# Performance work log

Hardware: AMD Instinct MI355X
Metric: run time of the kernel (lower is better)

The kernel has to match this reference:

```python
import jax, jax.numpy as jnp
import numpy as np

DIM = 1024
NUM_HEAD = 16
N_IMG = 64


def _linear_params(key, scale=0.02):
    kw, kb = jax.random.split(key)
    W = jax.random.normal(kw, (DIM, DIM), jnp.float32) * scale
    b = jax.random.normal(kb, (DIM,), jnp.float32) * scale
    return W, b


def setup_inputs() -> dict:
    key = jax.random.key(0)
    ks = jax.random.split(key, 5)
    # ragged per-image instance counts: 128..254, deterministic, sum = 12224
    lens = (128 + 2 * np.arange(N_IMG)).astype(np.int64)
    N = int(lens.sum())  # 12224
    x = jax.random.normal(ks[0], (N, DIM), jnp.float32)
    Wq, bq = _linear_params(ks[1])
    Wk, bk = _linear_params(ks[2])
    Wv, bv = _linear_params(ks[3])
    Wu, bu = _linear_params(ks[4])
    return {"x": x, "Wq": Wq, "bq": bq, "Wk": Wk, "bk": bk,
            "Wv": Wv, "bv": bv, "Wu": Wu, "bu": bu,
            "num_inst_per_image": jnp.asarray(lens)}


def _segment_layout(num_inst_per_image):
    # static (int) metadata -> numpy; returns padded gather idx, key mask, unpad idx
    lens = np.asarray(num_inst_per_image)
    B = lens.shape[0]
    L = int(lens.max())
    offsets = np.concatenate([[0], np.cumsum(lens)[:-1]])
    pos = offsets[:, None] + np.arange(L)[None, :]           # [B, L] flat positions
    valid = np.arange(L)[None, :] < lens[:, None]            # [B, L]
    gather_idx = jnp.asarray(np.where(valid, pos, 0))        # safe gather
    flat_take = jnp.asarray(np.flatnonzero(valid.ravel()))   # [N] unpad (row-major = segment order)
    return gather_idx, jnp.asarray(valid), flat_take, B, L


def reference(x, Wq, bq, Wk, bk, Wv, bv, Wu, bu, num_inst_per_image):
    gather_idx, valid, flat_take, B, L = _segment_layout(num_inst_per_image)
    N, C = x.shape
    H = NUM_HEAD
    D = C // H
    # global QKV projections on the flat batch (as in the torch module)
    q = (x @ Wq + bq)[gather_idx].reshape(B, L, H, D)
    k = (x @ Wk + bk)[gather_idx].reshape(B, L, H, D)
    v = (x @ Wv + bv)[gather_idx].reshape(B, L, H, D)
    scale = 1.0 / np.sqrt(C)  # note: original divides by sqrt(C), not sqrt(head_dim)
    attn = jnp.einsum('bqhd,bkhd->bhqk', q, k) * scale       # [B, H, L, L]
    bias = jnp.where(valid[:, None, None, :], 0.0, -jnp.inf)  # mask padded keys
    attn = jax.nn.softmax(attn + bias, axis=-1)
    out = jnp.einsum('bhqk,bkhd->bqhd', attn, v).reshape(B * L, C)
    out = out[flat_take]                                      # unpad back to [N, C]
    return out @ Wu + bu
```

## Files before the change

kernel.cpp:

```cpp
#include <hip/hip_runtime.h>
#include <hip/hip_bf16.h>
#include <math.h>

#define DIMC 1024
#define NHEAD 16
#define HDIM 64
#define MPAD 12288

using bf16x8 = __attribute__((ext_vector_type(8))) short;
using f32x4  = __attribute__((ext_vector_type(4))) float;
using f32x16 = __attribute__((ext_vector_type(16))) float;

__device__ inline ushort f2bf(float f) {
    uint u = __float_as_uint(f);
    u += 0x7fffu + ((u >> 16) & 1u);
    return (ushort)(u >> 16);
}
__device__ inline float bf2f(ushort h) { return __uint_as_float(((uint)h) << 16); }

__device__ inline uint pkbf(float a, float b) {
    __hip_bfloat162 t = __float22bfloat162_rn(float2{a, b});
    return *reinterpret_cast<uint*>(&t);
}

__device__ inline void gload_lds16(const ushort* g, ushort* l) {
    __builtin_amdgcn_global_load_lds(
        (const __attribute__((address_space(1))) uint*)g,
        (__attribute__((address_space(3))) uint*)l, 16, 0, 0);
}

__global__ __launch_bounds__(512, 4) void gemm192(
    const ushort* __restrict__ A, const ushort* __restrict__ Bt,
    const float* __restrict__ bq, const float* __restrict__ bk,
    const float* __restrict__ bv,
    ushort* __restrict__ qb, ushort* __restrict__ kb, ushort* __restrict__ vb,
    int M)
{
    __shared__ ushort lds[2][(128 + 192) * 64];

    const int bid = blockIdx.x;
    const int xcd = bid & 7;
    const int j   = bid >> 3;
    const int mt  = xcd * 12 + (j % 12);
    const int nt  = j / 12;
    const int row0 = mt * 128;
    const int col0 = nt * 192;

    const int t512 = threadIdx.x;
    const int w    = t512 >> 6;
    const int lane = t512 & 63;
    const int wm   = w >> 2;
    const int wn   = w & 3;
    const int l15  = lane & 15;
    const int kh   = lane >> 4;

    const int a0row = (w < 4) ? (w * 8) : (64 + (w - 4) * 8);
    const int a1row = a0row + 32;

    auto stage = [&](int buf, int kt, int mat, int relRow) {
        const int o   = relRow * 128 + lane * 16;
        const int row = o >> 7;
        const int kb_ = (o & 127) ^ ((row & 7) << 4);
        const ushort* src = (mat ? Bt + (size_t)(col0 + row) * DIMC
                                 : A  + (size_t)(row0 + row) * DIMC)
                            + kt * 64 + (kb_ >> 1);
        gload_lds16(src, &lds[buf][0] + mat * (128 * 64) + relRow * 64);
    };
    auto rdA = [&](int buf, int rf, int ks) -> bf16x8 {
        const int row = wm * 64 + rf * 16 + l15;
        const int ad  = (row * 128 + ks * 64 + kh * 16) ^ ((row & 7) << 4);
        return *(const bf16x8*)(&lds[buf][0] + (ad >> 1));
    };
    auto rdB = [&](int buf, int n, int ks) -> bf16x8 {
        const int row = wn * 48 + n * 16 + l15;
        const int ad  = (row * 128 + ks * 64 + kh * 16) ^ ((row & 7) << 4);
        return *(const bf16x8*)(&lds[buf][128 * 64] + (ad >> 1));
    };

    f32x4 acc[4][3] = {};
    bf16x8 af[2][2];
    bf16x8 bf[3][2];

    stage(0, 0, 0, a0row);
    stage(0, 0, 1, w * 24);
    stage(0, 0, 1, w * 24 + 8);
    stage(0, 0, 1, w * 24 + 16);
    stage(0, 0, 0, a1row);

    const int NT = DIMC / 64;
    for (int t = 0; t < NT; ++t) {
        const int cur = t & 1;
        const int nxt = cur ^ 1;
        const int tn  = (t + 1 < NT) ? (t + 1) : (NT - 1);

        asm volatile("s_waitcnt vmcnt(1)" ::: "memory");
        __builtin_amdgcn_s_barrier();
        __builtin_amdgcn_sched_barrier(0);
        #pragma unroll
        for (int rf = 0; rf < 2; ++rf)
            #pragma unroll
            for (int ks = 0; ks < 2; ++ks)
                af[rf][ks] = rdA(cur, rf, ks);
        #pragma unroll
        for (int n = 0; n < 3; ++n)
            #pragma unroll
            for (int ks = 0; ks < 2; ++ks)
                bf[n][ks] = rdB(cur, n, ks);
        stage(nxt, tn, 0, a0row);
        stage(nxt, tn, 1, w * 24);
        stage(nxt, tn, 1, w * 24 + 8);
        stage(nxt, tn, 1, w * 24 + 16);
        __builtin_amdgcn_s_setprio(1);
        #pragma unroll
        for (int rf = 0; rf < 2; ++rf)
            #pragma unroll
            for (int n = 0; n < 3; ++n)
                #pragma unroll
                for (int ks = 0; ks < 2; ++ks)
                    acc[rf][n] = __builtin_amdgcn_mfma_f32_16x16x32_bf16(
                        af[rf][ks], bf[n][ks], acc[rf][n], 0, 0, 0);
        __builtin_amdgcn_s_setprio(0);

        asm volatile("s_waitcnt vmcnt(4)" ::: "memory");
        __builtin_amdgcn_s_barrier();
        __builtin_amdgcn_sched_barrier(0);
        #pragma unroll
        for (int rf = 0; rf < 2; ++rf)
            #pragma unroll
            for (int ks = 0; ks < 2; ++ks)
                af[rf][ks] = rdA(cur, 2 + rf, ks);
        stage(nxt, tn, 0, a1row);
        __builtin_amdgcn_s_setprio(1);
        #pragma unroll
        for (int rf = 0; rf < 2; ++rf)
            #pragma unroll
            for (int n = 0; n < 3; ++n)
                #pragma unroll
                for (int ks = 0; ks < 2; ++ks)
                    acc[2 + rf][n] = __builtin_amdgcn_mfma_f32_16x16x32_bf16(
                        af[rf][ks], bf[n][ks], acc[2 + rf][n], 0, 0, 0);
        __builtin_amdgcn_s_setprio(0);
    }

    #pragma unroll
    for (int n = 0; n < 3; ++n) {
        const int cg = col0 + wn * 48 + n * 16 + l15;
        const int s  = cg >> 10;
        const int cb = cg & 1023;
        const float bb = ((s == 0) ? bq : (s == 1) ? bk : bv)[cb];
        ushort* op     = (s == 0) ? qb : (s == 1) ? kb : vb;
        #pragma unroll
        for (int i = 0; i < 4; ++i) {
            #pragma unroll
            for (int r = 0; r < 4; ++r) {
                const int gr = row0 + wm * 64 + i * 16 + kh * 4 + r;
                if (gr < M)
                    op[(size_t)gr * DIMC + cb] = f2bf(acc[i][n][r] + bb);
            }
        }
    }
}

__global__ __launch_bounds__(512, 4) void gemmF(
    const ushort* __restrict__ A, const ushort* __restrict__ Bt,
    const float* __restrict__ bias, float* __restrict__ C, int M)
{
    __shared__ ushort lds[2][(192 + 128) * 64];

    const int bid = blockIdx.x;
    const int xcd = bid & 7;
    const int j   = bid >> 3;
    const int mt  = xcd * 8 + (j % 8);
    const int nt  = j / 8;
    const int row0 = mt * 192;
    const int col0 = nt * 128;

    const int t512 = threadIdx.x;
    const int w    = t512 >> 6;
    const int lane = t512 & 63;
    const int wm   = w >> 1;
    const int wn   = w & 1;
    const int l15  = lane & 15;
    const int kh   = lane >> 4;

    auto stage = [&](int buf, int kt, int mat, int relRow) {
        const int o   = relRow * 128 + lane * 16;
        const int row = o >> 7;
        const int kb_ = (o & 127) ^ ((row & 7) << 4);
        const ushort* src = (mat ? Bt + (size_t)(col0 + row) * DIMC
                                 : A  + (size_t)(row0 + row) * DIMC)
                            + kt * 64 + (kb_ >> 1);
        gload_lds16(src, &lds[buf][0] + mat * (192 * 64) + relRow * 64);
    };
    auto rdA = [&](int buf, int rf, int ks) -> bf16x8 {
        const int row = wm * 48 + rf * 16 + l15;
        const int ad  = (row * 128 + ks * 64 + kh * 16) ^ ((row & 7) << 4);
        return *(const bf16x8*)(&lds[buf][0] + (ad >> 1));
    };
    auto rdB = [&](int buf, int n, int ks) -> bf16x8 {
        const int row = wn * 64 + n * 16 + l15;
        const int ad  = (row * 128 + ks * 64 + kh * 16) ^ ((row & 7) << 4);
        return *(const bf16x8*)(&lds[buf][192 * 64] + (ad >> 1));
    };

    f32x4 acc[3][4] = {};
    bf16x8 af[3][2];
    bf16x8 bf[4][2];

    stage(0, 0, 1, w * 16);
    stage(0, 0, 1, w * 16 + 8);
    stage(0, 0, 0, w * 8);
    stage(0, 0, 0, 64 + w * 8);
    stage(0, 0, 0, 128 + w * 8);

    const int NT = DIMC / 64;
    for (int t = 0; t < NT; ++t) {
        const int cur = t & 1;
        const int nxt = cur ^ 1;
        const int tn  = (t + 1 < NT) ? (t + 1) : (NT - 1);

        asm volatile("s_waitcnt vmcnt(0)" ::: "memory");
        __builtin_amdgcn_s_barrier();
        __builtin_amdgcn_sched_barrier(0);

        #pragma unroll
        for (int rf = 0; rf < 3; ++rf)
            #pragma unroll
            for (int ks = 0; ks < 2; ++ks)
                af[rf][ks] = rdA(cur, rf, ks);
        #pragma unroll
        for (int n = 0; n < 4; ++n)
            #pragma unroll
            for (int ks = 0; ks < 2; ++ks)
                bf[n][ks] = rdB(cur, n, ks);

        stage(nxt, tn, 1, w * 16);
        stage(nxt, tn, 1, w * 16 + 8);
        stage(nxt, tn, 0, w * 8);
        stage(nxt, tn, 0, 64 + w * 8);
        stage(nxt, tn, 0, 128 + w * 8);

        __builtin_amdgcn_s_setprio(1);
        #pragma unroll
        for (int rf = 0; rf < 3; ++rf)
            #pragma unroll
            for (int n = 0; n < 4; ++n)
                #pragma unroll
                for (int ks = 0; ks < 2; ++ks)
                    acc[rf][n] = __builtin_amdgcn_mfma_f32_16x16x32_bf16(
                        af[rf][ks], bf[n][ks], acc[rf][n], 0, 0, 0);
        __builtin_amdgcn_s_setprio(0);
    }

    #pragma unroll
    for (int n = 0; n < 4; ++n) {
        const int c  = col0 + wn * 64 + n * 16 + l15;
        const float bb = bias[c];
        #pragma unroll
        for (int i = 0; i < 3; ++i) {
            #pragma unroll
            for (int r = 0; r < 4; ++r) {
                const int gr = row0 + wm * 48 + i * 16 + kh * 4 + r;
                if (gr < M)
                    C[(size_t)gr * DIMC + c] = acc[i][n][r] + bb;
            }
        }
    }
}

__global__ __launch_bounds__(256) void cvt_pad(
    const float* __restrict__ x, ushort* __restrict__ xb, int nvalid, int ntot)
{
    const int stride = gridDim.x * blockDim.x;
    for (int i = blockIdx.x * blockDim.x + threadIdx.x; i < ntot / 4; i += stride) {
        const int e = i * 4;
        ushort4 o;
        if (e < nvalid) {
            const float4 f = *(const float4*)(x + e);
            o.x = f2bf(f.x); o.y = f2bf(f.y); o.z = f2bf(f.z); o.w = f2bf(f.w);
        } else { o.x = o.y = o.z = o.w = 0; }
        *(ushort4*)(xb + e) = o;
    }
}

__global__ __launch_bounds__(256) void transpose_w4(
    const float* __restrict__ W0, const float* __restrict__ W1,
    const float* __restrict__ W2, const float* __restrict__ W3,
    ushort* __restrict__ T0, ushort* __restrict__ T1,
    ushort* __restrict__ T2, ushort* __restrict__ T3)
{
    __shared__ float tile[32][33];
    const int z = blockIdx.z;
    const float* W = (z == 0) ? W0 : (z == 1) ? W1 : (z == 2) ? W2 : W3;
    ushort*      T = (z == 0) ? T0 : (z == 1) ? T1 : (z == 2) ? T2 : T3;
    const int tx = threadIdx.x & 31;
    const int ty = threadIdx.x >> 5;
    const int n0 = blockIdx.x * 32;
    const int k0 = blockIdx.y * 32;
    #pragma unroll
    for (int i = 0; i < 32; i += 8)
        tile[ty + i][tx] = W[(size_t)(k0 + ty + i) * DIMC + n0 + tx];
    __syncthreads();
    #pragma unroll
    for (int i = 0; i < 32; i += 8)
        T[(size_t)(n0 + ty + i) * DIMC + k0 + tx] = f2bf(tile[tx][ty + i]);
}

__global__ __launch_bounds__(256) void attn_mfma(
    const ushort* __restrict__ qg, const ushort* __restrict__ kg,
    const ushort* __restrict__ vg, ushort* __restrict__ og,
    const int* __restrict__ lens, int B)
{
    __shared__ ushort Kt[2][64 * 64];
    __shared__ ushort Vt[64 * 68];

    const int i   = blockIdx.x;
    const int xcd = i & 7;
    const int j   = i >> 3;
    const int bh  = xcd * (B * 2) + j;
    const int h   = bh & 15;
    const int b   = bh >> 4;

    const int tid  = threadIdx.x;
    const int qt   = tid >> 6;
    const int lane = tid & 63;

    const int myl = (lane < B) ? lens[lane] : 0;
    int inc = myl;
    #pragma unroll
    for (int d = 1; d < 64; d <<= 1) {
        const int nb = __shfl_up(inc, d);
        if (lane >= d) inc += nb;
    }
    const int off = __shfl(inc, b) - __shfl(myl, b);
    const int L   = __shfl(myl, b);
    const int ntk = (L + 63) >> 6;
    const bool active = (qt * 64 < L);

    const int l31 = lane & 31;
    const int hi  = lane >> 5;

    bf16x8 qf[2][4];
    if (active) {
        #pragma unroll
        for (int qn = 0; qn < 2; ++qn) {
            const size_t row = (size_t)(off + min(qt * 64 + qn * 32 + l31, L - 1));
            #pragma unroll
            for (int ks = 0; ks < 4; ++ks) {
                union { uint4 u4; ushort us[8]; bf16x8 v; } tmp;
                tmp.u4 = *(const uint4*)(qg + row * DIMC + h * HDIM + ks * 16 + hi * 8);
                #pragma unroll
                for (int e = 0; e < 8; ++e)
                    tmp.us[e] = f2bf(bf2f(tmp.us[e]) * 0.03125f);
                qf[qn][ks] = tmp.v;
            }
        }
    }

    auto stageK = [&](int tt, int buf) {
        #pragma unroll
        for (int u0 = 0; u0 < 2; ++u0) {
            const int u   = tid + u0 * 256;
            const int o   = u * 16;
            const int row = o >> 7;
            const int kb_ = (o & 127) ^ ((row & 7) << 4);
            const ushort* src = kg + (size_t)(off + min(tt * 64 + row, L - 1)) * DIMC
                                + h * HDIM + (kb_ >> 1);
            gload_lds16(src, &Kt[buf][0] + u * 8);
        }
    };

    const int pr   = lane & 7;
    const int doct = lane >> 3;
    const int d0v  = doct * 8;
    uint4 v0, v1;
    auto loadV = [&](int tt) {
        const int k0 = tt * 64 + qt * 16 + 2 * pr;
        v0 = *(const uint4*)(vg + (size_t)(off + min(k0,     L - 1)) * DIMC + h * HDIM + d0v);
        v1 = *(const uint4*)(vg + (size_t)(off + min(k0 + 1, L - 1)) * DIMC + h * HDIM + d0v);
    };

    stageK(0, 0);
    loadV(0);

    f32x16 o[2][2] = {};
    float mst[2] = {-1e30f, -1e30f};
    float lst[2] = {0.f, 0.f};

    for (int t = 0; t < ntk; ++t) {
        const int cur = t & 1;
        const int j0  = t * 64;
        const int tn  = (t + 1 < ntk) ? (t + 1) : (ntk - 1);

        stageK(tn, cur ^ 1);
        asm volatile("s_waitcnt vmcnt(2)" ::: "memory");
        __builtin_amdgcn_s_barrier();
        __builtin_amdgcn_sched_barrier(0);

        f32x16 s[2][2] = {};
        if (active) {
            bf16x8 kf[2][4];
            #pragma unroll
            for (int km = 0; km < 2; ++km) {
                const int row = km * 32 + l31;
                #pragma unroll
                for (int ks = 0; ks < 4; ++ks) {
                    const int ad = (row * 128 + ks * 32 + hi * 16) ^ ((row & 7) << 4);
                    kf[km][ks] = *(const bf16x8*)(&Kt[cur][0] + (ad >> 1));
                }
            }
            __builtin_amdgcn_s_setprio(1);
            #pragma unroll
            for (int km = 0; km < 2; ++km)
                #pragma unroll
                for (int qn = 0; qn < 2; ++qn)
                    #pragma unroll
                    for (int ks = 0; ks < 4; ++ks)
                        s[km][qn] = __builtin_amdgcn_mfma_f32_32x32x16_bf16(
                            kf[km][ks], qf[qn][ks], s[km][qn], 0, 0, 0);
            __builtin_amdgcn_s_setprio(0);
        }

        {
            const uint a4[4] = {v0.x, v0.y, v0.z, v0.w};
            const uint b4[4] = {v1.x, v1.y, v1.z, v1.w};
            const int  col   = qt * 16 + 2 * pr;
            #pragma unroll
            for (int jj = 0; jj < 4; ++jj) {
                const uint lo  = (a4[jj] & 0xffffu) | (b4[jj] << 16);
                const uint hi2 = (a4[jj] >> 16) | (b4[jj] & 0xffff0000u);
                *(uint*)&Vt[(d0v + 2 * jj)     * 68 + col] = lo;
                *(uint*)&Vt[(d0v + 2 * jj + 1) * 68 + col] = hi2;
            }
        }
        if (t + 1 < ntk) loadV(t + 1);

        if (active) {
            const bool fullTile = (j0 + 64 <= L);
            float tmv[2];
            #pragma unroll
            for (int qn = 0; qn < 2; ++qn) {
                float tm = -1e30f;
                if (fullTile) {
                    #pragma unroll
                    for (int km = 0; km < 2; ++km)
                        #pragma unroll
                        for (int r = 0; r < 16; ++r)
                            tm = fmaxf(tm, s[km][qn][r]);
                } else {
                    #pragma unroll
                    for (int km = 0; km < 2; ++km)
                        #pragma unroll
                        for (int r = 0; r < 16; ++r) {
                            const int key = j0 + km * 32 + (r & 3) + 8 * (r >> 2) + 4 * hi;
                            float sv = s[km][qn][r];
                            sv = (key < L) ? sv : -1e30f;
                            s[km][qn][r] = sv;
                            tm = fmaxf(tm, sv);
                        }
                }
                tm = fmaxf(tm, __shfl_xor(tm, 32));
                tmv[qn] = tm;
            }

            const bool need = (tmv[0] > mst[0] + 4.f) || (tmv[1] > mst[1] + 4.f);
            if (__any(need)) {
                #pragma unroll
                for (int qn = 0; qn < 2; ++qn) {
                    const float nm = fmaxf(mst[qn], tmv[qn]);
                    const float corr = __expf(mst[qn] - nm);
                    mst[qn] = nm;
                    lst[qn] *= corr;
                    #pragma unroll
                    for (int dm = 0; dm < 2; ++dm)
                        #pragma unroll
                        for (int r = 0; r < 16; ++r)
                            o[dm][qn][r] *= corr;
                }
            }
            #pragma unroll
            for (int qn = 0; qn < 2; ++qn) {
                float ls = 0.f;
                #pragma unroll
                for (int km = 0; km < 2; ++km)
                    #pragma unroll
                    for (int r = 0; r < 16; ++r) {
                        const float p = __expf(s[km][qn][r] - mst[qn]);
                        s[km][qn][r] = p;
                        ls += p;
                    }
                ls += __shfl_xor(ls, 32);
                lst[qn] += ls;
            }
        }

        asm volatile("s_waitcnt lgkmcnt(0)" ::: "memory");
        __builtin_amdgcn_s_barrier();
        __builtin_amdgcn_sched_barrier(0);

        if (active) {
            #pragma unroll
            for (int kspv = 0; kspv < 4; ++kspv) {
                const int km = kspv >> 1;
                const int sb = kspv & 1;

                bf16x8 Afr[2];
                #pragma unroll
                for (int dm = 0; dm < 2; ++dm) {
                    const int d = dm * 32 + l31;
                    const uint2 p0 = *(const uint2*)&Vt[d * 68 + kspv * 16 + hi * 8];
                    const uint2 p1 = *(const uint2*)&Vt[d * 68 + kspv * 16 + hi * 8 + 4];
                    union { uint u[4]; bf16x8 v; } aa;
                    aa.u[0] = p0.x; aa.u[1] = p0.y; aa.u[2] = p1.x; aa.u[3] = p1.y;
                    Afr[dm] = aa.v;
                }

                bf16x8 Bfr[2];
                #pragma unroll
                for (int qn = 0; qn < 2; ++qn) {
                    const uint X0 = pkbf(s[km][qn][8 * sb + 0], s[km][qn][8 * sb + 1]);
                    const uint X1 = pkbf(s[km][qn][8 * sb + 2], s[km][qn][8 * sb + 3]);
                    const uint Y0 = pkbf(s[km][qn][8 * sb + 4], s[km][qn][8 * sb + 5]);
                    const uint Y1 = pkbf(s[km][qn][8 * sb + 6], s[km][qn][8 * sb + 7]);
                    const uint sx0 = (uint)__shfl_xor((int)X0, 32);
                    const uint sx1 = (uint)__shfl_xor((int)X1, 32);
                    const uint sy0 = (uint)__shfl_xor((int)Y0, 32);
                    const uint sy1 = (uint)__shfl_xor((int)Y1, 32);
                    union { uint u[4]; bf16x8 v; } bb;
                    bb.u[0] = hi ? sy0 : X0;
                    bb.u[1] = hi ? sy1 : X1;
                    bb.u[2] = hi ? Y0 : sx0;
                    bb.u[3] = hi ? Y1 : sx1;
                    Bfr[qn] = bb.v;
                }

                __builtin_amdgcn_s_setprio(1);
                #pragma unroll
                for (int dm = 0; dm < 2; ++dm)
                    #pragma unroll
                    for (int qn = 0; qn < 2; ++qn)
                        o[dm][qn] = __builtin_amdgcn_mfma_f32_32x32x16_bf16(
                            Afr[dm], Bfr[qn], o[dm][qn], 0, 0, 0);
                __builtin_amdgcn_s_setprio(0);
            }
        }
    }

    if (active) {
        #pragma unroll
        for (int qn = 0; qn < 2; ++qn) {
            const int q = qt * 64 + qn * 32 + l31;
            if (q < L) {
                const float inv = 1.f / lst[qn];
                ushort* orow = og + (size_t)(off + q) * DIMC + h * HDIM;
                #pragma unroll
                for (int dm = 0; dm < 2; ++dm)
                    #pragma unroll
                    for (int bq2 = 0; bq2 < 4; ++bq2) {
                        const int r0 = 4 * bq2;
                        uint2 st;
                        st.x = pkbf(o[dm][qn][r0 + 0] * inv, o[dm][qn][r0 + 1] * inv);
                        st.y = pkbf(o[dm][qn][r0 + 2] * inv, o[dm][qn][r0 + 3] * inv);
                        *(uint2*)(orow + dm * 32 + 8 * bq2 + 4 * hi) = st;
                    }
            }
        }
    }
}

extern "C" void kernel_launch(void* const* d_in, const int* in_sizes, int n_in,
                              void* d_out, int out_size, void* d_ws, size_t ws_size,
                              hipStream_t stream)
{
    const float* x   = (const float*)d_in[0];
    const float* Wq  = (const float*)d_in[1];
    const float* bq  = (const float*)d_in[2];
    const float* Wk  = (const float*)d_in[3];
    const float* bk  = (const float*)d_in[4];
    const float* Wv  = (const float*)d_in[5];
    const float* bv  = (const float*)d_in[6];
    const float* Wu  = (const float*)d_in[7];
    const float* bu  = (const float*)d_in[8];
    const int*  lens = (const int*)d_in[9];

    const int N = in_sizes[0] / DIMC;
    const int B = in_sizes[9];

    ushort* xb  = (ushort*)d_ws;
    ushort* wtq = xb  + (size_t)MPAD * DIMC;
    ushort* wtk = wtq + (size_t)DIMC * DIMC;
    ushort* wtv = wtk + (size_t)DIMC * DIMC;
    ushort* wtu = wtv + (size_t)DIMC * DIMC;
    ushort* kb  = wtu + (size_t)DIMC * DIMC;
    ushort* vb  = kb  + (size_t)N * DIMC;
    ushort* qb  = (ushort*)d_out;
    ushort* ob  = xb;

    cvt_pad<<<2048, 256, 0, stream>>>(x, xb, N * DIMC, MPAD * DIMC);
    transpose_w4<<<dim3(32, 32, 4), 256, 0, stream>>>(Wq, Wk, Wv, Wu,
                                                      wtq, wtk, wtv, wtu);

    gemm192<<<1536, 512, 0, stream>>>(xb, wtq, bq, bk, bv, qb, kb, vb, N);

    attn_mfma<<<dim3(B * NHEAD), dim3(256), 0, stream>>>(qb, kb, vb, ob, lens, B);

    gemmF<<<512, 512, 0, stream>>>(ob, wtu, bu, (float*)d_out, N);
}
```

Measured before the change: 243.6 us.

## Split GEMM k-tile into three A-row phases with partial vmcnt waits

The GEMM main loop now processes each A sub-tile row block in three separate phases. Each phase waits only for its own A rows with a partial vmcnt, then barriers, reads its fragment and issues its MFMAs, so global-to-LDS staging of later row blocks overlaps compute on earlier ones. Staging assignments are remapped so each wave pair loads the row blocks it needs in phase order. A fragment registers drop from six to two, in exchange for three barriers per k-tile instead of one and tighter reliance on correct vmcnt counts.

```diff
diff --git a/kernel.cpp b/kernel.cpp
--- a/kernel.cpp
+++ b/kernel.cpp
@@ -204,14 +204,18 @@
     };
 
     f32x4 acc[3][4] = {};
-    bf16x8 af[3][2];
+    bf16x8 af[2];
     bf16x8 bf[4][2];
+
+    const int aP0 = wm * 48 + wn * 8;
+    const int aP1 = aP0 + 16;
+    const int aP2 = aP0 + 32;
 
     stage(0, 0, 1, w * 16);
     stage(0, 0, 1, w * 16 + 8);
-    stage(0, 0, 0, w * 8);
-    stage(0, 0, 0, 64 + w * 8);
-    stage(0, 0, 0, 128 + w * 8);
+    stage(0, 0, 0, aP0);
+    stage(0, 0, 0, aP1);
+    stage(0, 0, 0, aP2);
 
     const int NT = DIMC / 64;
     for (int t = 0; t < NT; ++t) {
@@ -219,36 +223,59 @@
         const int nxt = cur ^ 1;
         const int tn  = (t + 1 < NT) ? (t + 1) : (NT - 1);
 
-        asm volatile("s_waitcnt vmcnt(0)" ::: "memory");
+        asm volatile("s_waitcnt vmcnt(2)" ::: "memory");
         __builtin_amdgcn_s_barrier();
         __builtin_amdgcn_sched_barrier(0);
-
-        #pragma unroll
-        for (int rf = 0; rf < 3; ++rf)
-            #pragma unroll
-            for (int ks = 0; ks < 2; ++ks)
-                af[rf][ks] = rdA(cur, rf, ks);
+        #pragma unroll
+        for (int ks = 0; ks < 2; ++ks)
+            af[ks] = rdA(cur, 0, ks);
         #pragma unroll
         for (int n = 0; n < 4; ++n)
             #pragma unroll
             for (int ks = 0; ks < 2; ++ks)
                 bf[n][ks] = rdB(cur, n, ks);
-
         stage(nxt, tn, 1, w * 16);
         stage(nxt, tn, 1, w * 16 + 8);
-        stage(nxt, tn, 0, w * 8);
-        stage(nxt, tn, 0, 64 + w * 8);
-        stage(nxt, tn, 0, 128 + w * 8);
-
+        stage(nxt, tn, 0, aP0);
         __builtin_amdgcn_s_setprio(1);
         #pragma unroll
-        for (int rf = 0; rf < 3; ++rf)
-            #pragma unroll
-            for (int n = 0; n < 4; ++n)
-                #pragma unroll
-                for (int ks = 0; ks < 2; ++ks)
-                    acc[rf][n] = __builtin_amdgcn_mfma_f32_16x16x32_bf16(
-                        af[rf][ks], bf[n][ks], acc[rf][n], 0, 0, 0);
+        for (int n = 0; n < 4; ++n)
+            #pragma unroll
+            for (int ks = 0; ks < 2; ++ks)
+                acc[0][n] = __builtin_amdgcn_mfma_f32_16x16x32_bf16(
+                    af[ks], bf[n][ks], acc[0][n], 0, 0, 0);
+        __builtin_amdgcn_s_setprio(0);
+
+        asm volatile("s_waitcnt vmcnt(4)" ::: "memory");
+        __builtin_amdgcn_s_barrier();
+        __builtin_amdgcn_sched_barrier(0);
+        #pragma unroll
+        for (int ks = 0; ks < 2; ++ks)
+            af[ks] = rdA(cur, 1, ks);
+        stage(nxt, tn, 0, aP1);
+        __builtin_amdgcn_s_setprio(1);
+        #pragma unroll
+        for (int n = 0; n < 4; ++n)
+            #pragma unroll
+            for (int ks = 0; ks < 2; ++ks)
+                acc[1][n] = __builtin_amdgcn_mfma_f32_16x16x32_bf16(
+                    af[ks], bf[n][ks], acc[1][n], 0, 0, 0);
+        __builtin_amdgcn_s_setprio(0);
+
+        asm volatile("s_waitcnt vmcnt(4)" ::: "memory");
+        __builtin_amdgcn_s_barrier();
+        __builtin_amdgcn_sched_barrier(0);
+        #pragma unroll
+        for (int ks = 0; ks < 2; ++ks)
+            af[ks] = rdA(cur, 2, ks);
+        stage(nxt, tn, 0, aP2);
+        __builtin_amdgcn_s_setprio(1);
+        #pragma unroll
+        for (int n = 0; n < 4; ++n)
+            #pragma unroll
+            for (int ks = 0; ks < 2; ++ks)
+                acc[2][n] = __builtin_amdgcn_mfma_f32_16x16x32_bf16(
+                    af[ks], bf[n][ks], acc[2][n], 0, 0, 0);
         __builtin_amdgcn_s_setprio(0);
     }
 
```

Result: faster. 221.5 us (-9.1%).
